# Optimization experiments

Hardware: AMD Instinct MI355X
Metric: run time of the kernel (lower is better)

The kernel has to match this reference:

```python
import jax, jax.numpy as jnp
import numpy as np

INPUT_SIZE = 1024
HEAD_SIZE = 64


def setup_inputs() -> dict:
    key = jax.random.key(0)
    kx, kk, kq, kv = jax.random.split(key, 4)
    B, T, C, H = 4, 4096, INPUT_SIZE, HEAD_SIZE
    x = jax.random.normal(kx, (B, T, C), dtype=jnp.float32)
    # nn.Linear(C, H, bias=False) weight is (H, C); we store transposed (C, H)
    # so that y = x @ W matches torch's x @ weight.T
    scale = 1.0 / np.sqrt(C)
    Wk = jax.random.uniform(kk, (C, H), dtype=jnp.float32, minval=-scale, maxval=scale)
    Wq = jax.random.uniform(kq, (C, H), dtype=jnp.float32, minval=-scale, maxval=scale)
    Wv = jax.random.uniform(kv, (C, H), dtype=jnp.float32, minval=-scale, maxval=scale)
    return {"x": x, "Wk": Wk, "Wq": Wq, "Wv": Wv}


def reference(x, Wk, Wq, Wv):
    B, T, C = x.shape
    k = x @ Wk  # (B, T, H)
    q = x @ Wq
    v = x @ Wv
    H = k.shape[-1]
    # scaled scores (B, T, T)
    wei = jnp.einsum('bth,bsh->bts', q, k) * (H ** -0.5)
    causal = jnp.tril(jnp.ones((T, T), dtype=bool))
    wei = jnp.where(causal, wei, -jnp.inf)
    wei = jax.nn.softmax(wei, axis=-1)
    out = jnp.einsum('bts,bsh->bth', wei, v)  # (B, T, H)
    return out
```

## Files before the change

kernel.cpp:

```cpp
#include <hip/hip_runtime.h>
#include <math.h>


#define BT   16384
#define TDIM 4096
#define CDIM 1024
#define HDIM 64
#define ACCW 68

typedef __attribute__((ext_vector_type(8))) short bf16x8;
typedef __attribute__((ext_vector_type(4))) float f32x4;
typedef __attribute__((ext_vector_type(8))) unsigned short us8;
typedef __attribute__((ext_vector_type(4))) unsigned short us4;

static __device__ __forceinline__ unsigned short f2bf(float f) {
    unsigned int u = __float_as_uint(f);
    u += 0x7fffu + ((u >> 16) & 1u);
    return (unsigned short)(u >> 16);
}

__global__ __launch_bounds__(256) void wtrans_zero(
    const float* __restrict__ Wk, const float* __restrict__ Wq,
    const float* __restrict__ Wv, unsigned short* __restrict__ wtg,
    float* __restrict__ accp)
{
    int idx = blockIdx.x * 256 + threadIdx.x;
    int mat = idx >> 16;
    int rem = idx & 65535;
    int h = rem >> 10, c = rem & 1023;
    const float* W = (mat == 0) ? Wk : (mat == 1) ? Wq : Wv;
    wtg[idx] = f2bf(W[c * HDIM + h]);
    for (int i = idx; i < BT * ACCW; i += 196608) accp[i] = 0.f;
}

__global__ __launch_bounds__(512) void qkv_proj(
    const float* __restrict__ x, const unsigned short* __restrict__ wtg,
    unsigned short* __restrict__ kg, unsigned short* __restrict__ qg,
    unsigned short* __restrict__ vtg)
{
    __shared__ __align__(16) unsigned short xs[32][72];
    __shared__ __align__(16) unsigned short wts[192][72];
    const int t = threadIdx.x;
    const int lane = t & 63, wv = t >> 6, quad = lane >> 4, l16 = lane & 15;
    const int mt = wv >> 2;
    const int nq = wv & 3;
    const int row0 = blockIdx.x * 32;

    const int xr = t >> 4, xc4 = (t & 15) * 4;
    const int wn = t >> 3, wc8 = (t & 7) * 8;

    f32x4 acc3[3];
    #pragma unroll
    for (int i = 0; i < 3; i++) acc3[i] = (f32x4){0.f, 0.f, 0.f, 0.f};

    float4 xv = *(const float4*)&x[(size_t)(row0 + xr) * CDIM + xc4];
    us8 w0 = *(const us8*)&wtg[(size_t)(wn +   0) * CDIM + wc8];
    us8 w1 = *(const us8*)&wtg[(size_t)(wn +  64) * CDIM + wc8];
    us8 w2 = *(const us8*)&wtg[(size_t)(wn + 128) * CDIM + wc8];

    for (int cc = 0; cc < CDIM; cc += 64) {
        __syncthreads();
        us4 pk = { f2bf(xv.x), f2bf(xv.y), f2bf(xv.z), f2bf(xv.w) };
        *(us4*)&xs[xr][xc4] = pk;
        *(us8*)&wts[wn +   0][wc8] = w0;
        *(us8*)&wts[wn +  64][wc8] = w1;
        *(us8*)&wts[wn + 128][wc8] = w2;
        __syncthreads();
        if (cc + 64 < CDIM) {
            int nc = cc + 64;
            xv = *(const float4*)&x[(size_t)(row0 + xr) * CDIM + nc + xc4];
            w0 = *(const us8*)&wtg[(size_t)(wn +   0) * CDIM + nc + wc8];
            w1 = *(const us8*)&wtg[(size_t)(wn +  64) * CDIM + nc + wc8];
            w2 = *(const us8*)&wtg[(size_t)(wn + 128) * CDIM + nc + wc8];
        }
        bf16x8 a0 = *(const bf16x8*)&xs[mt * 16 + l16][quad * 8];
        bf16x8 a1 = *(const bf16x8*)&xs[mt * 16 + l16][32 + quad * 8];
        #pragma unroll
        for (int j = 0; j < 3; j++) {
            int nt = nq * 3 + j;
            bf16x8 b0 = *(const bf16x8*)&wts[nt * 16 + l16][quad * 8];
            bf16x8 b1 = *(const bf16x8*)&wts[nt * 16 + l16][32 + quad * 8];
            acc3[j] = __builtin_amdgcn_mfma_f32_16x16x32_bf16(a0, b0, acc3[j], 0, 0, 0);
            acc3[j] = __builtin_amdgcn_mfma_f32_16x16x32_bf16(a1, b1, acc3[j], 0, 0, 0);
        }
    }

    const int mrow = row0 + mt * 16 + quad * 4;
    #pragma unroll
    for (int j = 0; j < 3; j++) {
        int nt = nq * 3 + j;
        int mat = nt >> 2;
        int col = (nt & 3) * 16 + l16;
        #pragma unroll
        for (int reg = 0; reg < 4; reg++) {
            int r = mrow + reg;
            unsigned short bv = f2bf(acc3[j][reg]);
            if (mat == 0)      kg[(size_t)r * HDIM + col] = bv;
            else if (mat == 1) qg[(size_t)r * HDIM + col] = bv;
            else {
                int bb = r >> 12, tr = r & 4095;
                vtg[((size_t)(bb * HDIM + col) << 12) + tr] = bv;
            }
        }
    }
}

__global__ __launch_bounds__(256) void attn(
    const unsigned short* __restrict__ qg, const unsigned short* __restrict__ kg,
    const unsigned short* __restrict__ vtg, float* __restrict__ accp)
{
    __shared__ __align__(16) unsigned short Ks[64][72];
    __shared__ __align__(16) unsigned short Vt[80][72];
    __shared__ __align__(16) unsigned short Ps[4][16][72];

    const int t = threadIdx.x;
    const int lane = t & 63, wv = t >> 6, quad = lane >> 4, l16 = lane & 15;

    const int b = blockIdx.x / 160;
    const int s = blockIdx.x - b * 160;
    int qt, c;
    if (s < 16)      { qt = s;               c = 0; }
    else if (s < 48) { int u = s - 16; qt = 16 + (u >> 1); c = u & 1; }
    else if (s < 96) { int u = s - 48; int q3 = u / 3; qt = 32 + q3; c = u - 3 * q3; }
    else             { int u = s - 96; qt = 48 + (u >> 2); c = u & 3; }

    const size_t bbase = (size_t)b * TDIM;
    const int Q0 = qt * 64;
    const int kt0 = c * 16;
    const int kt1 = (kt0 + 15 < qt) ? kt0 + 15 : qt;

    for (int i = t; i < 16 * 72; i += 256) {
        int r = i / 72, cc = i - r * 72;
        Vt[64 + r][cc] = (r == 0) ? (unsigned short)0x3F80 : (unsigned short)0;
    }

    const int qrow = Q0 + wv * 16 + l16;
    bf16x8 qa0 = *(const bf16x8*)&qg[(bbase + qrow) * HDIM + quad * 8];
    bf16x8 qa1 = *(const bf16x8*)&qg[(bbase + qrow) * HDIM + 32 + quad * 8];

    f32x4 O[5];
    #pragma unroll
    for (int i = 0; i < 5; i++) O[i] = (f32x4){0.f, 0.f, 0.f, 0.f};

    const int fr = t >> 3, fc = (t & 7) * 8;

    us8 kr0 = *(const us8*)&kg[(bbase + kt0 * 64 + fr) * HDIM + fc];
    us8 kr1 = *(const us8*)&kg[(bbase + kt0 * 64 + fr + 32) * HDIM + fc];
    us8 vr0 = *(const us8*)&vtg[((size_t)(b * HDIM + fr) << 12) + kt0 * 64 + fc];
    us8 vr1 = *(const us8*)&vtg[((size_t)(b * HDIM + fr + 32) << 12) + kt0 * 64 + fc];

    const int rbase = wv * 16 + quad * 4;
    for (int kt = kt0; kt <= kt1; kt++) {
        __syncthreads();
        *(us8*)&Ks[fr][fc] = kr0;
        *(us8*)&Ks[fr + 32][fc] = kr1;
        *(us8*)&Vt[fr][fc] = vr0;
        *(us8*)&Vt[fr + 32][fc] = vr1;
        __syncthreads();
        if (kt < kt1) {
            int kn = kt + 1;
            kr0 = *(const us8*)&kg[(bbase + kn * 64 + fr) * HDIM + fc];
            kr1 = *(const us8*)&kg[(bbase + kn * 64 + fr + 32) * HDIM + fc];
            vr0 = *(const us8*)&vtg[((size_t)(b * HDIM + fr) << 12) + kn * 64 + fc];
            vr1 = *(const us8*)&vtg[((size_t)(b * HDIM + fr + 32) << 12) + kn * 64 + fc];
        }

        f32x4 sT[4];
        #pragma unroll
        for (int st = 0; st < 4; st++) {
            bf16x8 kb0 = *(const bf16x8*)&Ks[st * 16 + l16][quad * 8];
            bf16x8 kb1 = *(const bf16x8*)&Ks[st * 16 + l16][32 + quad * 8];
            f32x4 z = (f32x4){0.f, 0.f, 0.f, 0.f};
            z = __builtin_amdgcn_mfma_f32_16x16x32_bf16(qa0, kb0, z, 0, 0, 0);
            z = __builtin_amdgcn_mfma_f32_16x16x32_bf16(qa1, kb1, z, 0, 0, 0);
            sT[st] = z;
        }
        const bool diag = (kt == qt);
        #pragma unroll
        for (int st = 0; st < 4; st++) {
            int col = st * 16 + l16;
            #pragma unroll
            for (int r = 0; r < 4; r++) {
                float p = (diag && (col > rbase + r)) ? 0.f
                                                      : __expf(sT[st][r] * 0.125f);
                Ps[wv][quad * 4 + r][col] = f2bf(p);
            }
        }
        bf16x8 pa0 = *(const bf16x8*)&Ps[wv][l16][quad * 8];
        bf16x8 pa1 = *(const bf16x8*)&Ps[wv][l16][32 + quad * 8];
        #pragma unroll
        for (int nt = 0; nt < 5; nt++) {
            bf16x8 vb0 = *(const bf16x8*)&Vt[nt * 16 + l16][quad * 8];
            bf16x8 vb1 = *(const bf16x8*)&Vt[nt * 16 + l16][32 + quad * 8];
            O[nt] = __builtin_amdgcn_mfma_f32_16x16x32_bf16(pa0, vb0, O[nt], 0, 0, 0);
            O[nt] = __builtin_amdgcn_mfma_f32_16x16x32_bf16(pa1, vb1, O[nt], 0, 0, 0);
        }
    }

    const int grow = (b << 12) + Q0 + wv * 16 + quad * 4;
    #pragma unroll
    for (int nt = 0; nt < 4; nt++)
        #pragma unroll
        for (int r = 0; r < 4; r++)
            atomicAdd(&accp[(size_t)(grow + r) * ACCW + nt * 16 + l16], O[nt][r]);
    if (l16 == 0) {
        #pragma unroll
        for (int r = 0; r < 4; r++)
            atomicAdd(&accp[(size_t)(grow + r) * ACCW + 64], O[4][r]);
    }
}

__global__ __launch_bounds__(256) void normalize(
    const float* __restrict__ accp, float* __restrict__ out)
{
    int idx = blockIdx.x * 256 + threadIdx.x;
    int row = idx >> 4, c4 = (idx & 15) * 4;
    float inv = 1.f / accp[(size_t)row * ACCW + 64];
    float4 o = *(const float4*)&accp[(size_t)row * ACCW + c4];
    float4 res = make_float4(o.x * inv, o.y * inv, o.z * inv, o.w * inv);
    *(float4*)&out[(size_t)row * HDIM + c4] = res;
}

extern "C" void kernel_launch(void* const* d_in, const int* in_sizes, int n_in,
                              void* d_out, int out_size, void* d_ws, size_t ws_size,
                              hipStream_t stream) {
    const float* x  = (const float*)d_in[0];
    const float* Wk = (const float*)d_in[1];
    const float* Wq = (const float*)d_in[2];
    const float* Wv = (const float*)d_in[3];
    float* out = (float*)d_out;

    unsigned short* wtg = (unsigned short*)d_ws;
    unsigned short* kg  = wtg + 196608;
    unsigned short* qg  = kg + (size_t)BT * HDIM;
    unsigned short* vtg = qg + (size_t)BT * HDIM;
    float* accp = (float*)(vtg + (size_t)4 * HDIM * TDIM);

    wtrans_zero<<<768, 256, 0, stream>>>(Wk, Wq, Wv, wtg, accp);
    qkv_proj<<<BT / 32, 512, 0, stream>>>(x, wtg, kg, qg, vtg);
    attn<<<4 * 160, 256, 0, stream>>>(qg, kg, vtg, accp);
    normalize<<<BT * HDIM / (4 * 256), 256, 0, stream>>>(accp, out);
}
```

Before: 147.7 us.

## Enlarge attention query tile to 128 rows, fold scale into Q, restructure projection

The attention kernel now gives each wave 32 query rows (128 per block) so every K/V tile loaded into shared memory feeds twice as many MFMAs. The split is re-partitioned to 144 blocks per batch, each covering up to 8 key tiles. The softmax scale and log2(e) are folded into Q at projection time so the inner loop uses exp2f, and masking writes -1e30 only on diagonal tiles. The projection kernel reads weights directly from global/L2 instead of staging them in LDS, the weight transpose is rewritten for coalesced reads, and accumulator zeroing moves to hipMemsetAsync. These cut redundant K/V traffic and exp work, at the cost of more registers per thread and uncached global weight loads.

```diff
diff --git a/kernel.cpp b/kernel.cpp
--- a/kernel.cpp
+++ b/kernel.cpp
@@ -7,6 +7,7 @@
 #define CDIM 1024
 #define HDIM 64
 #define ACCW 68
+#define QSCALE 0.18033688f
 
 typedef __attribute__((ext_vector_type(8))) short bf16x8;
 typedef __attribute__((ext_vector_type(4))) float f32x4;
@@ -19,18 +20,16 @@
     return (unsigned short)(u >> 16);
 }
 
-__global__ __launch_bounds__(256) void wtrans_zero(
+__global__ __launch_bounds__(256) void wtrans(
     const float* __restrict__ Wk, const float* __restrict__ Wq,
-    const float* __restrict__ Wv, unsigned short* __restrict__ wtg,
-    float* __restrict__ accp)
+    const float* __restrict__ Wv, unsigned short* __restrict__ wtg)
 {
     int idx = blockIdx.x * 256 + threadIdx.x;
     int mat = idx >> 16;
     int rem = idx & 65535;
-    int h = rem >> 10, c = rem & 1023;
+    int h = rem & 63, c = rem >> 6;
     const float* W = (mat == 0) ? Wk : (mat == 1) ? Wq : Wv;
-    wtg[idx] = f2bf(W[c * HDIM + h]);
-    for (int i = idx; i < BT * ACCW; i += 196608) accp[i] = 0.f;
+    wtg[(size_t)(mat * 64 + h) * CDIM + c] = f2bf(W[c * HDIM + h]);
 }
 
 __global__ __launch_bounds__(512) void qkv_proj(
@@ -39,47 +38,34 @@
     unsigned short* __restrict__ vtg)
 {
     __shared__ __align__(16) unsigned short xs[32][72];
-    __shared__ __align__(16) unsigned short wts[192][72];
     const int t = threadIdx.x;
     const int lane = t & 63, wv = t >> 6, quad = lane >> 4, l16 = lane & 15;
     const int mt = wv >> 2;
     const int nq = wv & 3;
     const int row0 = blockIdx.x * 32;
-
     const int xr = t >> 4, xc4 = (t & 15) * 4;
-    const int wn = t >> 3, wc8 = (t & 7) * 8;
 
     f32x4 acc3[3];
     #pragma unroll
     for (int i = 0; i < 3; i++) acc3[i] = (f32x4){0.f, 0.f, 0.f, 0.f};
 
     float4 xv = *(const float4*)&x[(size_t)(row0 + xr) * CDIM + xc4];
-    us8 w0 = *(const us8*)&wtg[(size_t)(wn +   0) * CDIM + wc8];
-    us8 w1 = *(const us8*)&wtg[(size_t)(wn +  64) * CDIM + wc8];
-    us8 w2 = *(const us8*)&wtg[(size_t)(wn + 128) * CDIM + wc8];
 
     for (int cc = 0; cc < CDIM; cc += 64) {
         __syncthreads();
         us4 pk = { f2bf(xv.x), f2bf(xv.y), f2bf(xv.z), f2bf(xv.w) };
         *(us4*)&xs[xr][xc4] = pk;
-        *(us8*)&wts[wn +   0][wc8] = w0;
-        *(us8*)&wts[wn +  64][wc8] = w1;
-        *(us8*)&wts[wn + 128][wc8] = w2;
-        __syncthreads();
-        if (cc + 64 < CDIM) {
-            int nc = cc + 64;
-            xv = *(const float4*)&x[(size_t)(row0 + xr) * CDIM + nc + xc4];
-            w0 = *(const us8*)&wtg[(size_t)(wn +   0) * CDIM + nc + wc8];
-            w1 = *(const us8*)&wtg[(size_t)(wn +  64) * CDIM + nc + wc8];
-            w2 = *(const us8*)&wtg[(size_t)(wn + 128) * CDIM + nc + wc8];
-        }
+        __syncthreads();
+        if (cc + 64 < CDIM)
+            xv = *(const float4*)&x[(size_t)(row0 + xr) * CDIM + cc + 64 + xc4];
+
         bf16x8 a0 = *(const bf16x8*)&xs[mt * 16 + l16][quad * 8];
         bf16x8 a1 = *(const bf16x8*)&xs[mt * 16 + l16][32 + quad * 8];
         #pragma unroll
         for (int j = 0; j < 3; j++) {
             int nt = nq * 3 + j;
-            bf16x8 b0 = *(const bf16x8*)&wts[nt * 16 + l16][quad * 8];
-            bf16x8 b1 = *(const bf16x8*)&wts[nt * 16 + l16][32 + quad * 8];
+            bf16x8 b0 = *(const bf16x8*)&wtg[(size_t)(nt * 16 + l16) * CDIM + cc + quad * 8];
+            bf16x8 b1 = *(const bf16x8*)&wtg[(size_t)(nt * 16 + l16) * CDIM + cc + 32 + quad * 8];
             acc3[j] = __builtin_amdgcn_mfma_f32_16x16x32_bf16(a0, b0, acc3[j], 0, 0, 0);
             acc3[j] = __builtin_amdgcn_mfma_f32_16x16x32_bf16(a1, b1, acc3[j], 0, 0, 0);
         }
@@ -94,7 +80,9 @@
         #pragma unroll
         for (int reg = 0; reg < 4; reg++) {
             int r = mrow + reg;
-            unsigned short bv = f2bf(acc3[j][reg]);
+            float val = acc3[j][reg];
+            if (mat == 1) val *= QSCALE;
+            unsigned short bv = f2bf(val);
             if (mat == 0)      kg[(size_t)r * HDIM + col] = bv;
             else if (mat == 1) qg[(size_t)r * HDIM + col] = bv;
             else {
@@ -105,42 +93,50 @@
     }
 }
 
-__global__ __launch_bounds__(256) void attn(
+__global__ __launch_bounds__(256, 3) void attn(
     const unsigned short* __restrict__ qg, const unsigned short* __restrict__ kg,
     const unsigned short* __restrict__ vtg, float* __restrict__ accp)
 {
     __shared__ __align__(16) unsigned short Ks[64][72];
     __shared__ __align__(16) unsigned short Vt[80][72];
-    __shared__ __align__(16) unsigned short Ps[4][16][72];
+    __shared__ __align__(16) unsigned short Ps[4][32][72];
 
     const int t = threadIdx.x;
     const int lane = t & 63, wv = t >> 6, quad = lane >> 4, l16 = lane & 15;
 
-    const int b = blockIdx.x / 160;
-    const int s = blockIdx.x - b * 160;
-    int qt, c;
-    if (s < 16)      { qt = s;               c = 0; }
-    else if (s < 48) { int u = s - 16; qt = 16 + (u >> 1); c = u & 1; }
-    else if (s < 96) { int u = s - 48; int q3 = u / 3; qt = 32 + q3; c = u - 3 * q3; }
-    else             { int u = s - 96; qt = 48 + (u >> 2); c = u & 3; }
+    const int b = blockIdx.x / 144;
+    int s = blockIdx.x - b * 144;
+    int g = 0;
+    while (2 * (g + 1) * (g + 2) <= s) g++;
+    int u = s - 2 * g * (g + 1);
+    int qi = 4 * g + u / (g + 1);
+    int c  = u - (u / (g + 1)) * (g + 1);
 
     const size_t bbase = (size_t)b * TDIM;
-    const int Q0 = qt * 64;
-    const int kt0 = c * 16;
-    const int kt1 = (kt0 + 15 < qt) ? kt0 + 15 : qt;
+    const int Q0 = qi * 128;
+    const int ktmax = 2 * qi + 1;
+    const int kt0 = c * 8;
+    const int kt1 = (kt0 + 7 < ktmax) ? kt0 + 7 : ktmax;
 
     for (int i = t; i < 16 * 72; i += 256) {
         int r = i / 72, cc = i - r * 72;
         Vt[64 + r][cc] = (r == 0) ? (unsigned short)0x3F80 : (unsigned short)0;
     }
 
-    const int qrow = Q0 + wv * 16 + l16;
-    bf16x8 qa0 = *(const bf16x8*)&qg[(bbase + qrow) * HDIM + quad * 8];
-    bf16x8 qa1 = *(const bf16x8*)&qg[(bbase + qrow) * HDIM + 32 + quad * 8];
-
-    f32x4 O[5];
-    #pragma unroll
-    for (int i = 0; i < 5; i++) O[i] = (f32x4){0.f, 0.f, 0.f, 0.f};
+    const int wrow0 = wv * 32;
+    bf16x8 qa[2][2];
+    #pragma unroll
+    for (int mt2 = 0; mt2 < 2; mt2++) {
+        size_t qr = bbase + Q0 + wrow0 + mt2 * 16 + l16;
+        qa[mt2][0] = *(const bf16x8*)&qg[qr * HDIM + quad * 8];
+        qa[mt2][1] = *(const bf16x8*)&qg[qr * HDIM + 32 + quad * 8];
+    }
+
+    f32x4 O[2][5];
+    #pragma unroll
+    for (int mt2 = 0; mt2 < 2; mt2++)
+        #pragma unroll
+        for (int i = 0; i < 5; i++) O[mt2][i] = (f32x4){0.f, 0.f, 0.f, 0.f};
 
     const int fr = t >> 3, fc = (t & 7) * 8;
 
@@ -149,7 +145,6 @@
     us8 vr0 = *(const us8*)&vtg[((size_t)(b * HDIM + fr) << 12) + kt0 * 64 + fc];
     us8 vr1 = *(const us8*)&vtg[((size_t)(b * HDIM + fr + 32) << 12) + kt0 * 64 + fc];
 
-    const int rbase = wv * 16 + quad * 4;
     for (int kt = kt0; kt <= kt1; kt++) {
         __syncthreads();
         *(us8*)&Ks[fr][fc] = kr0;
@@ -165,48 +160,73 @@
             vr1 = *(const us8*)&vtg[((size_t)(b * HDIM + fr + 32) << 12) + kn * 64 + fc];
         }
 
-        f32x4 sT[4];
+        f32x4 sT[2][4];
         #pragma unroll
         for (int st = 0; st < 4; st++) {
             bf16x8 kb0 = *(const bf16x8*)&Ks[st * 16 + l16][quad * 8];
             bf16x8 kb1 = *(const bf16x8*)&Ks[st * 16 + l16][32 + quad * 8];
-            f32x4 z = (f32x4){0.f, 0.f, 0.f, 0.f};
-            z = __builtin_amdgcn_mfma_f32_16x16x32_bf16(qa0, kb0, z, 0, 0, 0);
-            z = __builtin_amdgcn_mfma_f32_16x16x32_bf16(qa1, kb1, z, 0, 0, 0);
-            sT[st] = z;
-        }
-        const bool diag = (kt == qt);
-        #pragma unroll
-        for (int st = 0; st < 4; st++) {
-            int col = st * 16 + l16;
-            #pragma unroll
-            for (int r = 0; r < 4; r++) {
-                float p = (diag && (col > rbase + r)) ? 0.f
-                                                      : __expf(sT[st][r] * 0.125f);
-                Ps[wv][quad * 4 + r][col] = f2bf(p);
+            #pragma unroll
+            for (int mt2 = 0; mt2 < 2; mt2++) {
+                f32x4 z = (f32x4){0.f, 0.f, 0.f, 0.f};
+                z = __builtin_amdgcn_mfma_f32_16x16x32_bf16(qa[mt2][0], kb0, z, 0, 0, 0);
+                z = __builtin_amdgcn_mfma_f32_16x16x32_bf16(qa[mt2][1], kb1, z, 0, 0, 0);
+                sT[mt2][st] = z;
             }
         }
-        bf16x8 pa0 = *(const bf16x8*)&Ps[wv][l16][quad * 8];
-        bf16x8 pa1 = *(const bf16x8*)&Ps[wv][l16][32 + quad * 8];
+        if (kt * 64 + 63 > Q0 + wrow0) {
+            #pragma unroll
+            for (int mt2 = 0; mt2 < 2; mt2++)
+                #pragma unroll
+                for (int st = 0; st < 4; st++) {
+                    int gcol = kt * 64 + st * 16 + l16;
+                    #pragma unroll
+                    for (int r = 0; r < 4; r++) {
+                        int grow = Q0 + wrow0 + mt2 * 16 + quad * 4 + r;
+                        if (gcol > grow) sT[mt2][st][r] = -1e30f;
+                    }
+                }
+        }
+        #pragma unroll
+        for (int mt2 = 0; mt2 < 2; mt2++)
+            #pragma unroll
+            for (int st = 0; st < 4; st++)
+                #pragma unroll
+                for (int r = 0; r < 4; r++) {
+                    float p = exp2f(sT[mt2][st][r]);
+                    Ps[wv][mt2 * 16 + quad * 4 + r][st * 16 + l16] = f2bf(p);
+                }
+
+        bf16x8 pa[2][2];
+        #pragma unroll
+        for (int mt2 = 0; mt2 < 2; mt2++) {
+            pa[mt2][0] = *(const bf16x8*)&Ps[wv][mt2 * 16 + l16][quad * 8];
+            pa[mt2][1] = *(const bf16x8*)&Ps[wv][mt2 * 16 + l16][32 + quad * 8];
+        }
         #pragma unroll
         for (int nt = 0; nt < 5; nt++) {
             bf16x8 vb0 = *(const bf16x8*)&Vt[nt * 16 + l16][quad * 8];
             bf16x8 vb1 = *(const bf16x8*)&Vt[nt * 16 + l16][32 + quad * 8];
-            O[nt] = __builtin_amdgcn_mfma_f32_16x16x32_bf16(pa0, vb0, O[nt], 0, 0, 0);
-            O[nt] = __builtin_amdgcn_mfma_f32_16x16x32_bf16(pa1, vb1, O[nt], 0, 0, 0);
-        }
-    }
-
-    const int grow = (b << 12) + Q0 + wv * 16 + quad * 4;
-    #pragma unroll
-    for (int nt = 0; nt < 4; nt++)
-        #pragma unroll
-        for (int r = 0; r < 4; r++)
-            atomicAdd(&accp[(size_t)(grow + r) * ACCW + nt * 16 + l16], O[nt][r]);
-    if (l16 == 0) {
-        #pragma unroll
-        for (int r = 0; r < 4; r++)
-            atomicAdd(&accp[(size_t)(grow + r) * ACCW + 64], O[4][r]);
+            #pragma unroll
+            for (int mt2 = 0; mt2 < 2; mt2++) {
+                O[mt2][nt] = __builtin_amdgcn_mfma_f32_16x16x32_bf16(pa[mt2][0], vb0, O[mt2][nt], 0, 0, 0);
+                O[mt2][nt] = __builtin_amdgcn_mfma_f32_16x16x32_bf16(pa[mt2][1], vb1, O[mt2][nt], 0, 0, 0);
+            }
+        }
+    }
+
+    #pragma unroll
+    for (int mt2 = 0; mt2 < 2; mt2++) {
+        const int grow = (b << 12) + Q0 + wrow0 + mt2 * 16 + quad * 4;
+        #pragma unroll
+        for (int nt = 0; nt < 4; nt++)
+            #pragma unroll
+            for (int r = 0; r < 4; r++)
+                atomicAdd(&accp[(size_t)(grow + r) * ACCW + nt * 16 + l16], O[mt2][nt][r]);
+        if (l16 == 0) {
+            #pragma unroll
+            for (int r = 0; r < 4; r++)
+                atomicAdd(&accp[(size_t)(grow + r) * ACCW + 64], O[mt2][4][r]);
+        }
     }
 }
 
@@ -236,8 +256,9 @@
     unsigned short* vtg = qg + (size_t)BT * HDIM;
     float* accp = (float*)(vtg + (size_t)4 * HDIM * TDIM);
 
-    wtrans_zero<<<768, 256, 0, stream>>>(Wk, Wq, Wv, wtg, accp);
+    hipMemsetAsync(accp, 0, (size_t)BT * ACCW * sizeof(float), stream);
+    wtrans<<<768, 256, 0, stream>>>(Wk, Wq, Wv, wtg);
     qkv_proj<<<BT / 32, 512, 0, stream>>>(x, wtg, kg, qg, vtg);
-    attn<<<4 * 160, 256, 0, stream>>>(qg, kg, vtg, accp);
+    attn<<<4 * 144, 256, 0, stream>>>(qg, kg, vtg, accp);
     normalize<<<BT * HDIM / (4 * 256), 256, 0, stream>>>(accp, out);
 }
```

Measured after the change: 190.4 us. 1.29x slower.
